# Kernel tuning notes

Measured on AMD Instinct MI355X. Metric: run time of the kernel, lower is better.

Reference implementation:

```python
import jax, jax.numpy as jnp
import numpy as np

N_NODES = 100000
N_EDGES = 3200000


def _gcn_conv(x, W, b, src, dst, dinv, n_nodes):
    """PyG GCNConv: linear -> symmetric-normalized scatter-add over (self-looped) edges -> bias."""
    h = x @ W  # [N, out]
    norm = (dinv[src] * dinv[dst])[:, None]  # [E+N, 1]
    msg = h[src] * norm  # gather + scale
    out = jax.ops.segment_sum(msg, dst, num_segments=n_nodes)  # scatter-add
    return out + b


def setup_inputs() -> dict:
    key = jax.random.key(0)
    ks = jax.random.split(key, 16)
    x = jax.random.normal(ks[0], (N_NODES, 512), dtype=jnp.float32)
    edge_index = jax.random.randint(ks[1], (2, N_EDGES), 0, N_NODES, dtype=jnp.int32)

    def glorot(k, fan_in, fan_out):
        s = jnp.sqrt(6.0 / (fan_in + fan_out))
        return jax.random.uniform(k, (fan_in, fan_out), jnp.float32, -s, s)

    dims = [(512, 64), (64, 8), (8, 4), (4, 2), (4, 2)]
    names = ["1", "2", "3", "mu", "lv"]
    params = {}
    for i, ((fi, fo), nm) in enumerate(zip(dims, names)):
        params[f"W{nm}"] = glorot(ks[2 + i], fi, fo)
        params[f"b{nm}"] = jnp.zeros((fo,), jnp.float32)
    return {"x": x, "edge_index": edge_index, **params}


def reference(x, edge_index, W1, b1, W2, b2, W3, b3, Wmu, bmu, Wlv, blv):
    n = x.shape[0]
    loops = jnp.arange(n, dtype=edge_index.dtype)
    src = jnp.concatenate([edge_index[0], loops])  # add self-loops
    dst = jnp.concatenate([edge_index[1], loops])
    deg = jax.ops.segment_sum(jnp.ones_like(dst, dtype=x.dtype), dst, num_segments=n)
    dinv = jnp.where(deg > 0, jax.lax.rsqrt(jnp.maximum(deg, 1.0)), 0.0)

    h = jax.nn.relu(_gcn_conv(x, W1, b1, src, dst, dinv, n))
    h = jax.nn.relu(_gcn_conv(h, W2, b2, src, dst, dinv, n))
    h = jax.nn.relu(_gcn_conv(h, W3, b3, src, dst, dinv, n))
    mu = _gcn_conv(h, Wmu, bmu, src, dst, dinv, n)
    logvar = _gcn_conv(h, Wlv, blv, src, dst, dinv, n)
    return mu, logvar
```

## Files before the change

kernel.cpp:

```cpp
#include <hip/hip_runtime.h>
#include <hip/hip_fp16.h>
#include <stdint.h>


#define BSHIFT 7
#define BPB 128
#define CAP 5632
#define NBMAX 800
#define CAPB 40

typedef _Float16 f16x8 __attribute__((ext_vector_type(8)));
typedef float f32x4 __attribute__((ext_vector_type(4)));

__global__ __launch_bounds__(1024) void k_part(const int* __restrict__ esrc, const int* __restrict__ edst,
                                               int* __restrict__ bcnt, int* __restrict__ pairs,
                                               int E, int NB, int nblocks) {
  __shared__ int bincnt[NBMAX];
  __shared__ int sflushed[NBMAX];
  __shared__ int binbuf[NBMAX * CAPB];
  const int tid = threadIdx.x;
  for (int b = tid; b < NB; b += 1024) { bincnt[b] = 0; sflushed[b] = 0; }
  __syncthreads();
  const int chunk = (E + nblocks - 1) / nblocks;
  const int e0 = blockIdx.x * chunk;
  const int e1 = min(e0 + chunk, E);
  for (int base = e0; base < e1; base += 1024) {
    int e = base + tid;
    if (e < e1) {
      int d = edst[e], s = esrc[e];
      int b = d >> BSHIFT;
      int pos = atomicAdd(&bincnt[b], 1);
      binbuf[b * CAPB + (pos % CAPB)] = (s << BSHIFT) | (d & (BPB - 1));
    }
    __syncthreads();
    if (tid < NB) {
      int c = bincnt[tid], f = sflushed[tid];
      while (c - f >= 16) {
        int p = atomicAdd(&bcnt[tid * 16], 16);
#pragma unroll
        for (int j = 0; j < 16; ++j)
          pairs[(size_t)tid * CAP + p + j] = binbuf[tid * CAPB + ((f + j) % CAPB)];
        f += 16;
      }
      sflushed[tid] = f;
    }
    __syncthreads();
  }
  if (tid < NB) {
    int c = bincnt[tid], f = sflushed[tid];
    int rem = c - f;
    if (rem > 0) {
      int p = atomicAdd(&bcnt[tid * 16], rem);
      for (int j = 0; j < rem; ++j)
        pairs[(size_t)tid * CAP + p + j] = binbuf[tid * CAPB + ((f + j) % CAPB)];
    }
  }
}

__global__ __launch_bounds__(256) void k_wprep(const float* __restrict__ W, _Float16* __restrict__ wf) {
  int idx = blockIdx.x * 256 + threadIdx.x;
  int l = idx & 63, st = idx >> 6;
  int t = st & 3, s = st >> 2;
  int kg = l >> 4, c = l & 15;
  f16x8 v;
#pragma unroll
  for (int j = 0; j < 8; ++j)
    v[j] = (_Float16)W[(size_t)(s * 32 + kg * 8 + j) * 64 + t * 16 + c];
  *(f16x8*)(wf + (size_t)idx * 8) = v;
}

__global__ __launch_bounds__(256) void k_gemm1m(const float* __restrict__ x, const _Float16* __restrict__ wf,
                                                __half* __restrict__ h1, int n) {
  const int tid = threadIdx.x;
  const int lane = tid & 63;
  const int wv = tid >> 6;
  const int n0 = blockIdx.x * 128 + wv * 32;
  const int kg = lane >> 4;
  const int rr = lane & 15;

  const float* xr0 = x + (size_t)min(n0 + rr, n - 1) * 512 + kg * 8;
  const float* xr1 = x + (size_t)min(n0 + 16 + rr, n - 1) * 512 + kg * 8;
  const f16x8* wfp = (const f16x8*)wf + lane;

  float4 abuf[2][2][2];
  f16x8 wbuf[2][4];

  auto ldA = [&](float4 a[2][2], int t) {
    const int off = t * 32;
    a[0][0] = *(const float4*)(xr0 + off);
    a[0][1] = *(const float4*)(xr0 + off + 4);
    a[1][0] = *(const float4*)(xr1 + off);
    a[1][1] = *(const float4*)(xr1 + off + 4);
  };
  auto ldW = [&](f16x8 w[4], int t) {
#pragma unroll
    for (int j = 0; j < 4; ++j) w[j] = wfp[(t * 4 + j) * 64];
  };
  auto cvt8 = [&](const float4& lo, const float4& hi) -> f16x8 {
    f16x8 r;
    r[0] = (_Float16)lo.x; r[1] = (_Float16)lo.y; r[2] = (_Float16)lo.z; r[3] = (_Float16)lo.w;
    r[4] = (_Float16)hi.x; r[5] = (_Float16)hi.y; r[6] = (_Float16)hi.z; r[7] = (_Float16)hi.w;
    return r;
  };

  f32x4 acc[2][4];
#pragma unroll
  for (int m = 0; m < 2; ++m)
#pragma unroll
    for (int j = 0; j < 4; ++j) acc[m][j] = (f32x4){0.f, 0.f, 0.f, 0.f};

  ldA(abuf[0], 0);
  ldW(wbuf[0], 0);
#pragma unroll
  for (int t = 0; t < 16; ++t) {
    const int cur = t & 1, nxt = cur ^ 1;
    if (t + 1 < 16) {
      ldA(abuf[nxt], t + 1);
      ldW(wbuf[nxt], t + 1);
    }
    f16x8 am0 = cvt8(abuf[cur][0][0], abuf[cur][0][1]);
    f16x8 am1 = cvt8(abuf[cur][1][0], abuf[cur][1][1]);
#pragma unroll
    for (int j = 0; j < 4; ++j) {
      acc[0][j] = __builtin_amdgcn_mfma_f32_16x16x32_f16(am0, wbuf[cur][j], acc[0][j], 0, 0, 0);
      acc[1][j] = __builtin_amdgcn_mfma_f32_16x16x32_f16(am1, wbuf[cur][j], acc[1][j], 0, 0, 0);
    }
  }

#pragma unroll
  for (int m = 0; m < 2; ++m)
#pragma unroll
    for (int r = 0; r < 4; ++r) {
      int node = n0 + m * 16 + kg * 4 + r;
      if (node < n) {
#pragma unroll
        for (int j = 0; j < 4; ++j)
          h1[(size_t)node * 64 + j * 16 + rr] = __float2half_rn(acc[m][j][r]);
      }
    }
}

__global__ __launch_bounds__(1024) void k_bscan(const int* __restrict__ bcnt, int* __restrict__ bbase,
                                                int* __restrict__ offs, int NB, int n, int E) {
  __shared__ int sc[1024];
  int tid = threadIdx.x;
  int v = (tid < NB) ? bcnt[tid * 16] : 0;
  sc[tid] = v;
  __syncthreads();
  for (int d = 1; d < 1024; d <<= 1) {
    int t = (tid >= d) ? sc[tid - d] : 0;
    __syncthreads();
    if (tid >= d) sc[tid] += t;
    __syncthreads();
  }
  if (tid < NB) bbase[tid] = sc[tid] - v;
  if (tid == 0) offs[n] = E;
}

__global__ __launch_bounds__(1024) void k_p2(const int* __restrict__ pairs, const int* __restrict__ bcnt,
                                             const int* __restrict__ bbase, int* __restrict__ offs,
                                             float* __restrict__ dinv, int* __restrict__ csr, int n) {
  __shared__ int lcnt[BPB];
  __shared__ int scanv[BPB];
  __shared__ int cur[BPB];
  __shared__ int sbuf[CAP];
  const int tid = threadIdx.x;
  const int b = blockIdx.x;
  const int size = bcnt[b * 16];
  const int base = bbase[b];
  const int node0 = b << BSHIFT;
  const int nb = min(BPB, n - node0);

  if (tid < BPB) lcnt[tid] = 0;
  __syncthreads();

  int stash[6];
  int ns = 0;
  for (int i = tid; i < size; i += 1024) {
    int w = pairs[(size_t)b * CAP + i];
    stash[ns++] = w;
    atomicAdd(&lcnt[w & (BPB - 1)], 1);
  }
  __syncthreads();
  if (tid < BPB) scanv[tid] = lcnt[tid];
  __syncthreads();
#pragma unroll
  for (int d = 1; d < BPB; d <<= 1) {
    int t = (tid < BPB && tid >= d) ? scanv[tid - d] : 0;
    __syncthreads();
    if (tid < BPB && tid >= d) scanv[tid] += t;
    __syncthreads();
  }
  if (tid < nb) {
    int excl = scanv[tid] - lcnt[tid];
    offs[node0 + tid] = base + excl;
    cur[tid] = excl;
    dinv[node0 + tid] = rsqrtf((float)(lcnt[tid] + 1));
  }
  __syncthreads();
  for (int i = 0; i < ns; ++i) {
    int w = stash[i];
    int p = atomicAdd(&cur[w & (BPB - 1)], 1);
    sbuf[p] = w >> BSHIFT;
  }
  __syncthreads();
  for (int i = tid; i < size; i += 1024) csr[base + i] = sbuf[i];
}

__global__ __launch_bounds__(256) void k_pull64(const __half* __restrict__ h, const int* __restrict__ offs,
                                                const int* __restrict__ csr, const float* __restrict__ dinv,
                                                const float* __restrict__ b1, const float* __restrict__ W2,
                                                float* __restrict__ h2, int n) {
  __shared__ float sa[4][64];
  __shared__ float w2s[512];
  const int tid = threadIdx.x;
  w2s[tid] = W2[tid];
  w2s[tid + 256] = W2[tid + 256];
  const int lane = tid & 63;
  const int wv = tid >> 6;
  const int node = blockIdx.x * 4 + wv;
  float a1v = 0.f;
  if (node < n) {
    int s0 = offs[node], s1 = offs[node + 1];
    float di = dinv[node];
    float acc = 0.f;
    int e = s0;
    for (; e + 4 <= s1; e += 4) {
      int i0 = csr[e], i1 = csr[e + 1], i2 = csr[e + 2], i3 = csr[e + 3];
      float w0 = dinv[i0], w1 = dinv[i1], w2 = dinv[i2], w3 = dinv[i3];
      float v0 = __half2float(h[(size_t)i0 * 64 + lane]);
      float v1 = __half2float(h[(size_t)i1 * 64 + lane]);
      float v2 = __half2float(h[(size_t)i2 * 64 + lane]);
      float v3 = __half2float(h[(size_t)i3 * 64 + lane]);
      acc = fmaf(w0, v0, acc); acc = fmaf(w1, v1, acc);
      acc = fmaf(w2, v2, acc); acc = fmaf(w3, v3, acc);
    }
    for (; e < s1; ++e) {
      int s = csr[e];
      acc = fmaf(dinv[s], __half2float(h[(size_t)s * 64 + lane]), acc);
    }
    acc = fmaf(di, __half2float(h[(size_t)node * 64 + lane]), acc);
    a1v = fmaxf(fmaf(di, acc, b1[lane]), 0.f);
  }
  sa[wv][lane] = a1v;
  __syncthreads();
  if (tid < 32) {
    int j = tid >> 3, f = tid & 7;
    int nd = blockIdx.x * 4 + j;
    if (nd < n) {
      float s = 0.f;
#pragma unroll
      for (int l = 0; l < 64; ++l) s = fmaf(sa[j][l], w2s[l * 8 + f], s);
      h2[(size_t)nd * 8 + f] = s;
    }
  }
}

__global__ __launch_bounds__(256) void k_pull8(const float* __restrict__ h, const int* __restrict__ offs,
                                               const int* __restrict__ csr, const float* __restrict__ dinv,
                                               const float* __restrict__ b2, const float* __restrict__ W3,
                                               float* __restrict__ h3, int n) {
  __shared__ float sa[4][8];
  __shared__ float w3s[32];
  const int tid = threadIdx.x;
  if (tid < 32) w3s[tid] = W3[tid];
  const int lane = tid & 63;
  const int wv = tid >> 6;
  const int node = blockIdx.x * 4 + wv;
  const int j8 = lane >> 3, f = lane & 7;
  float pacc = 0.f;
  float di = 0.f;
  if (node < n) {
    int s0 = offs[node], s1 = offs[node + 1];
    di = dinv[node];
    for (int e0 = s0; e0 < s1; e0 += 8) {
      int e = e0 + j8;
      if (e < s1) {
        int s = csr[e];
        pacc = fmaf(dinv[s], h[(size_t)s * 8 + f], pacc);
      }
    }
  }
  pacc += __shfl_down(pacc, 32);
  pacc += __shfl_down(pacc, 16);
  pacc += __shfl_down(pacc, 8);
  if (node < n && lane < 8) {
    float v = pacc + di * h[(size_t)node * 8 + f];
    sa[wv][f] = fmaxf(fmaf(di, v, b2[f]), 0.f);
  }
  __syncthreads();
  if (tid < 16) {
    int j = tid >> 2, ff = tid & 3;
    int nd = blockIdx.x * 4 + j;
    if (nd < n) {
      float s = 0.f;
#pragma unroll
      for (int k = 0; k < 8; ++k) s = fmaf(sa[j][k], w3s[k * 4 + ff], s);
      h3[(size_t)nd * 4 + ff] = s;
    }
  }
}

__global__ __launch_bounds__(256) void k_pull4(const float* __restrict__ h, const int* __restrict__ offs,
                                               const int* __restrict__ csr, const float* __restrict__ dinv,
                                               const float* __restrict__ b3, float* __restrict__ out, int n) {
  const int tid = threadIdx.x;
  const int lane = tid & 63;
  const int node = blockIdx.x * 4 + (tid >> 6);
  if (node >= n) return;
  const int j16 = lane >> 2, f = lane & 3;
  int s0 = offs[node], s1 = offs[node + 1];
  float di = dinv[node];
  float pacc = 0.f;
  for (int e0 = s0; e0 < s1; e0 += 16) {
    int e = e0 + j16;
    if (e < s1) {
      int s = csr[e];
      pacc = fmaf(dinv[s], h[(size_t)s * 4 + f], pacc);
    }
  }
  pacc += __shfl_down(pacc, 32);
  pacc += __shfl_down(pacc, 16);
  pacc += __shfl_down(pacc, 8);
  pacc += __shfl_down(pacc, 4);
  if (lane < 4) {
    float v = pacc + di * h[(size_t)node * 4 + f];
    out[(size_t)node * 4 + f] = fmaxf(fmaf(di, v, b3[f]), 0.f);
  }
}

__global__ __launch_bounds__(256) void k_pull4o(const float* __restrict__ a3, const int* __restrict__ offs,
                                                const int* __restrict__ csr, const float* __restrict__ dinv,
                                                const float* __restrict__ Wmu, const float* __restrict__ bmu,
                                                const float* __restrict__ Wlv, const float* __restrict__ blv,
                                                float* __restrict__ outp, int n) {
  __shared__ float sg[4][4];
  const int tid = threadIdx.x;
  const int lane = tid & 63;
  const int wv = tid >> 6;
  const int node = blockIdx.x * 4 + wv;
  const int j16 = lane >> 2, f = lane & 3;
  float pacc = 0.f;
  float di = 0.f;
  if (node < n) {
    int s0 = offs[node], s1 = offs[node + 1];
    di = dinv[node];
    for (int e0 = s0; e0 < s1; e0 += 16) {
      int e = e0 + j16;
      if (e < s1) {
        int s = csr[e];
        pacc = fmaf(dinv[s], a3[(size_t)s * 4 + f], pacc);
      }
    }
  }
  pacc += __shfl_down(pacc, 32);
  pacc += __shfl_down(pacc, 16);
  pacc += __shfl_down(pacc, 8);
  pacc += __shfl_down(pacc, 4);
  if (node < n && lane < 4) {
    float v = pacc + di * a3[(size_t)node * 4 + f];
    sg[wv][f] = di * v;
  }
  __syncthreads();
  if (tid < 16) {
    int j = tid >> 2, c = tid & 3;
    int nd = blockIdx.x * 4 + j;
    if (nd < n) {
      const float* Wp = (c < 2) ? Wmu : Wlv;
      const float* bp = (c < 2) ? bmu : blv;
      int cc = c & 1;
      float s = bp[cc];
#pragma unroll
      for (int k = 0; k < 4; ++k) s = fmaf(sg[j][k], Wp[k * 2 + cc], s);
      size_t base = (c < 2) ? 0 : (size_t)2 * n;
      outp[base + (size_t)nd * 2 + cc] = s;
    }
  }
}

extern "C" void kernel_launch(void* const* d_in, const int* in_sizes, int n_in,
                              void* d_out, int out_size, void* d_ws, size_t ws_size,
                              hipStream_t stream) {
  const float* x = (const float*)d_in[0];
  const int* ei = (const int*)d_in[1];
  const float* W1 = (const float*)d_in[2];
  const float* b1 = (const float*)d_in[3];
  const float* W2 = (const float*)d_in[4];
  const float* b2 = (const float*)d_in[5];
  const float* W3 = (const float*)d_in[6];
  const float* b3 = (const float*)d_in[7];
  const float* Wmu = (const float*)d_in[8];
  const float* bmu = (const float*)d_in[9];
  const float* Wlv = (const float*)d_in[10];
  const float* blv = (const float*)d_in[11];
  float* out = (float*)d_out;

  const int N = in_sizes[0] / 512;
  const int E = in_sizes[1] / 2;
  const int* esrc = ei;
  const int* edst = ei + E;
  const int NB = (N + BPB - 1) >> BSHIFT;

  char* w = (char*)d_ws;
  size_t p = 0;
  auto alloc = [&](size_t bytes) -> void* {
    void* r = w + p;
    p = (p + bytes + 255) & ~(size_t)255;
    return r;
  };
  int* bcnt = (int*)alloc((size_t)NB * 16 * 4);
  int* bbase = (int*)alloc((size_t)NB * 4);
  int* offs = (int*)alloc((size_t)(N + 1) * 4);
  float* dinv = (float*)alloc((size_t)N * 4);
  int* csr = (int*)alloc((size_t)E * 4);
  int* pairs = (int*)alloc((size_t)NB * CAP * 4);
  __half* h1 = (__half*)alloc((size_t)N * 64 * 2);
  float* h2 = (float*)alloc((size_t)N * 8 * 4);
  float* h3 = (float*)alloc((size_t)N * 4 * 4);
  float* a3 = (float*)alloc((size_t)N * 4 * 4);
  _Float16* wf = (_Float16*)alloc((size_t)512 * 64 * 2);

  hipMemsetAsync(bcnt, 0, (size_t)NB * 16 * 4, stream);

  k_wprep<<<16, 256, 0, stream>>>(W1, wf);
  k_part<<<256, 1024, 0, stream>>>(esrc, edst, bcnt, pairs, E, NB, 256);
  k_gemm1m<<<(N + 127) / 128, 256, 0, stream>>>(x, wf, h1, N);
  k_bscan<<<1, 1024, 0, stream>>>(bcnt, bbase, offs, NB, N, E);
  k_p2<<<NB, 1024, 0, stream>>>(pairs, bcnt, bbase, offs, dinv, csr, N);

  k_pull64<<<(N + 3) / 4, 256, 0, stream>>>(h1, offs, csr, dinv, b1, W2, h2, N);
  k_pull8<<<(N + 3) / 4, 256, 0, stream>>>(h2, offs, csr, dinv, b2, W3, h3, N);
  k_pull4<<<(N + 3) / 4, 256, 0, stream>>>(h3, offs, csr, dinv, b3, a3, N);
  k_pull4o<<<(N + 3) / 4, 256, 0, stream>>>(a3, offs, csr, dinv, Wmu, bmu, Wlv, blv, out, N);
}
```

Before: 627.2 us.

## Fold source-side dinv scaling into producer outputs and vectorize 64-wide gather

```diff
diff --git a/kernel.cpp b/kernel.cpp
--- a/kernel.cpp
+++ b/kernel.cpp
@@ -70,7 +70,7 @@
 }
 
 __global__ __launch_bounds__(256) void k_gemm1m(const float* __restrict__ x, const _Float16* __restrict__ wf,
-                                                __half* __restrict__ h1, int n) {
+                                                const float* __restrict__ dinv, __half* __restrict__ h1, int n) {
   const int tid = threadIdx.x;
   const int lane = tid & 63;
   const int wv = tid >> 6;
@@ -133,9 +133,10 @@
     for (int r = 0; r < 4; ++r) {
       int node = n0 + m * 16 + kg * 4 + r;
       if (node < n) {
+        float di = dinv[node];
 #pragma unroll
         for (int j = 0; j < 4; ++j)
-          h1[(size_t)node * 64 + j * 16 + rr] = __float2half_rn(acc[m][j][r]);
+          h1[(size_t)node * 64 + j * 16 + rr] = __float2half_rn(di * acc[m][j][r]);
       }
     }
 }
@@ -211,7 +212,7 @@
                                                 const int* __restrict__ csr, const float* __restrict__ dinv,
                                                 const float* __restrict__ b1, const float* __restrict__ W2,
                                                 float* __restrict__ h2, int n) {
-  __shared__ float sa[4][64];
+  __shared__ float sa[4][65];
   __shared__ float w2s[512];
   const int tid = threadIdx.x;
   w2s[tid] = W2[tid];
@@ -219,30 +220,40 @@
   const int lane = tid & 63;
   const int wv = tid >> 6;
   const int node = blockIdx.x * 4 + wv;
-  float a1v = 0.f;
+  const int half = lane >> 5;
+  const int fp = lane & 31;
+  const uint32_t* hp = (const uint32_t*)h;
+  float ax = 0.f, ay = 0.f;
   if (node < n) {
-    int s0 = offs[node], s1 = offs[node + 1];
+    const int s0 = offs[node], s1 = offs[node + 1];
+    const int cnt = s1 - s0;
+    auto acc1 = [&](int srcnode) {
+      uint32_t v = hp[(size_t)srcnode * 32 + fp];
+      __half2 hv = *(__half2*)&v;
+      float2 f = __half22float2(hv);
+      ax += f.x; ay += f.y;
+    };
+    int base = 0;
+    for (; base + 8 <= cnt; base += 8) {
+      int e = s0 + base + half;
+      int i0 = csr[e], i1 = csr[e + 2], i2 = csr[e + 4], i3 = csr[e + 6];
+      acc1(i0); acc1(i1); acc1(i2); acc1(i3);
+    }
+    for (; base + 2 <= cnt; base += 2) {
+      int e = s0 + base + half;
+      acc1(csr[e]);
+    }
+    if (base < cnt && half == 0) acc1(csr[s0 + base]);
+    if (half == 1) acc1(node);
+  }
+  ax += __shfl_down(ax, 32);
+  ay += __shfl_down(ay, 32);
+  if (node < n && half == 0) {
     float di = dinv[node];
-    float acc = 0.f;
-    int e = s0;
-    for (; e + 4 <= s1; e += 4) {
-      int i0 = csr[e], i1 = csr[e + 1], i2 = csr[e + 2], i3 = csr[e + 3];
-      float w0 = dinv[i0], w1 = dinv[i1], w2 = dinv[i2], w3 = dinv[i3];
-      float v0 = __half2float(h[(size_t)i0 * 64 + lane]);
-      float v1 = __half2float(h[(size_t)i1 * 64 + lane]);
-      float v2 = __half2float(h[(size_t)i2 * 64 + lane]);
-      float v3 = __half2float(h[(size_t)i3 * 64 + lane]);
-      acc = fmaf(w0, v0, acc); acc = fmaf(w1, v1, acc);
-      acc = fmaf(w2, v2, acc); acc = fmaf(w3, v3, acc);
-    }
-    for (; e < s1; ++e) {
-      int s = csr[e];
-      acc = fmaf(dinv[s], __half2float(h[(size_t)s * 64 + lane]), acc);
-    }
-    acc = fmaf(di, __half2float(h[(size_t)node * 64 + lane]), acc);
-    a1v = fmaxf(fmaf(di, acc, b1[lane]), 0.f);
-  }
-  sa[wv][lane] = a1v;
+    float2 bb = *(const float2*)(b1 + 2 * fp);
+    sa[wv][2 * fp + 0] = fmaxf(fmaf(di, ax, bb.x), 0.f);
+    sa[wv][2 * fp + 1] = fmaxf(fmaf(di, ay, bb.y), 0.f);
+  }
   __syncthreads();
   if (tid < 32) {
     int j = tid >> 3, f = tid & 7;
@@ -251,7 +262,7 @@
       float s = 0.f;
 #pragma unroll
       for (int l = 0; l < 64; ++l) s = fmaf(sa[j][l], w2s[l * 8 + f], s);
-      h2[(size_t)nd * 8 + f] = s;
+      h2[(size_t)nd * 8 + f] = dinv[nd] * s;
     }
   }
 }
@@ -269,15 +280,13 @@
   const int node = blockIdx.x * 4 + wv;
   const int j8 = lane >> 3, f = lane & 7;
   float pacc = 0.f;
-  float di = 0.f;
   if (node < n) {
     int s0 = offs[node], s1 = offs[node + 1];
-    di = dinv[node];
     for (int e0 = s0; e0 < s1; e0 += 8) {
       int e = e0 + j8;
       if (e < s1) {
         int s = csr[e];
-        pacc = fmaf(dinv[s], h[(size_t)s * 8 + f], pacc);
+        pacc += h[(size_t)s * 8 + f];
       }
     }
   }
@@ -285,8 +294,8 @@
   pacc += __shfl_down(pacc, 16);
   pacc += __shfl_down(pacc, 8);
   if (node < n && lane < 8) {
-    float v = pacc + di * h[(size_t)node * 8 + f];
-    sa[wv][f] = fmaxf(fmaf(di, v, b2[f]), 0.f);
+    float v = pacc + h[(size_t)node * 8 + f];
+    sa[wv][f] = fmaxf(fmaf(dinv[node], v, b2[f]), 0.f);
   }
   __syncthreads();
   if (tid < 16) {
@@ -296,7 +305,7 @@
       float s = 0.f;
 #pragma unroll
       for (int k = 0; k < 8; ++k) s = fmaf(sa[j][k], w3s[k * 4 + ff], s);
-      h3[(size_t)nd * 4 + ff] = s;
+      h3[(size_t)nd * 4 + ff] = dinv[nd] * s;
     }
   }
 }
@@ -310,13 +319,12 @@
   if (node >= n) return;
   const int j16 = lane >> 2, f = lane & 3;
   int s0 = offs[node], s1 = offs[node + 1];
-  float di = dinv[node];
   float pacc = 0.f;
   for (int e0 = s0; e0 < s1; e0 += 16) {
     int e = e0 + j16;
     if (e < s1) {
       int s = csr[e];
-      pacc = fmaf(dinv[s], h[(size_t)s * 4 + f], pacc);
+      pacc += h[(size_t)s * 4 + f];
     }
   }
   pacc += __shfl_down(pacc, 32);
@@ -324,8 +332,9 @@
   pacc += __shfl_down(pacc, 8);
   pacc += __shfl_down(pacc, 4);
   if (lane < 4) {
-    float v = pacc + di * h[(size_t)node * 4 + f];
-    out[(size_t)node * 4 + f] = fmaxf(fmaf(di, v, b3[f]), 0.f);
+    float di = dinv[node];
+    float v = pacc + h[(size_t)node * 4 + f];
+    out[(size_t)node * 4 + f] = di * fmaxf(fmaf(di, v, b3[f]), 0.f);
   }
 }
 
@@ -341,15 +350,13 @@
   const int node = blockIdx.x * 4 + wv;
   const int j16 = lane >> 2, f = lane & 3;
   float pacc = 0.f;
-  float di = 0.f;
   if (node < n) {
     int s0 = offs[node], s1 = offs[node + 1];
-    di = dinv[node];
     for (int e0 = s0; e0 < s1; e0 += 16) {
       int e = e0 + j16;
       if (e < s1) {
         int s = csr[e];
-        pacc = fmaf(dinv[s], a3[(size_t)s * 4 + f], pacc);
+        pacc += a3[(size_t)s * 4 + f];
       }
     }
   }
@@ -358,8 +365,8 @@
   pacc += __shfl_down(pacc, 8);
   pacc += __shfl_down(pacc, 4);
   if (node < n && lane < 4) {
-    float v = pacc + di * a3[(size_t)node * 4 + f];
-    sg[wv][f] = di * v;
+    float v = pacc + a3[(size_t)node * 4 + f];
+    sg[wv][f] = dinv[node] * v;
   }
   __syncthreads();
   if (tid < 16) {
@@ -424,9 +431,9 @@
 
   k_wprep<<<16, 256, 0, stream>>>(W1, wf);
   k_part<<<256, 1024, 0, stream>>>(esrc, edst, bcnt, pairs, E, NB, 256);
-  k_gemm1m<<<(N + 127) / 128, 256, 0, stream>>>(x, wf, h1, N);
   k_bscan<<<1, 1024, 0, stream>>>(bcnt, bbase, offs, NB, N, E);
   k_p2<<<NB, 1024, 0, stream>>>(pairs, bcnt, bbase, offs, dinv, csr, N);
+  k_gemm1m<<<(N + 127) / 128, 256, 0, stream>>>(x, wf, dinv, h1, N);
 
   k_pull64<<<(N + 3) / 4, 256, 0, stream>>>(h1, offs, csr, dinv, b1, W2, h2, N);
   k_pull8<<<(N + 3) / 4, 256, 0, stream>>>(h2, offs, csr, dinv, b2, W3, h3, N);
```

New measurement: 587.2 us. -6.4%, faster.
